# Kernel optimization log

Measured on AMD Instinct MI355X. Metric: run time of the kernel, lower is better.

The kernel has to match this reference:

```python
import jax, jax.numpy as jnp
import numpy as np

VOCAB = 50257
EMBED = 256
NFREQ = 64
NRULES = 100
B, S = 4, 1024


def setup_inputs() -> dict:
    key = jax.random.key(0)
    ks = jax.random.split(key, 7)
    return {
        "token_ids": jax.random.randint(ks[0], (B, S), 0, VOCAB),
        "a_n": jax.random.normal(ks[1], (VOCAB, NFREQ), dtype=jnp.float32),
        "b_n": jax.random.normal(ks[2], (VOCAB, NFREQ), dtype=jnp.float32),
        "rule_transform": jax.random.normal(ks[3], (NRULES, EMBED, EMBED), dtype=jnp.float32),
        "token_rules": jax.random.randint(ks[4], (VOCAB,), 0, NRULES),
        "proj_w": jax.random.normal(ks[5], (EMBED, NFREQ), dtype=jnp.float32) * (1.0 / np.sqrt(NFREQ)),
        "proj_b": jax.random.normal(ks[6], (EMBED,), dtype=jnp.float32) * 0.01,
    }


def reference(token_ids, a_n, b_n, rule_transform, token_rules, proj_w, proj_b):
    vocab_size, nfreq = a_n.shape
    # fourier_freqs = linspace(1, F, F) -> [1..F]
    freqs = jnp.arange(1, nfreq + 1, dtype=jnp.float32)  # [F]
    x = token_ids.astype(jnp.float32)[..., None] / vocab_size  # [B,S,1]
    ang = (2.0 * jnp.pi) * freqs * x  # [B,S,F]
    # gather per-token fourier coefficients, fuse cos/sin combine
    fourier = a_n[token_ids] * jnp.cos(ang) + b_n[token_ids] * jnp.sin(ang)  # [B,S,F]
    base = jnp.einsum('bsf,df->bsd', fourier, proj_w) + proj_b  # [B,S,D]
    rule_idx = token_rules[token_ids]  # [B,S]
    rules = rule_transform[rule_idx]  # [B,S,D,D] gathered per token
    return jnp.einsum('bsd,bsde->bse', base, rules)  # [B,S,D]
```

## Files before the change

### kernel.cpp

```cpp
#include <hip/hip_runtime.h>
#include <math.h>

#define VOCAB   50257
#define EMBED   256
#define NFREQ   64
#define NRULES  100
#define NTOK    4096
#define CAP     256
#define CHUNK   16
#define NCHUNK  (CAP / CHUNK)

#define BASE_BYTES ((size_t)NTOK * EMBED * 4)
#define LIST_BYTES ((size_t)NRULES * CAP * 4)

__global__ __launch_bounds__(256) void prep_kernel(
    const float* __restrict__ proj_w,
    float*       __restrict__ wT,
    int*         __restrict__ counts)
{
    __shared__ float s_t[64 * 65];
    const int tid = threadIdx.x;
    const int b   = blockIdx.x;

    if (b == 0 && tid < NRULES) counts[tid] = 0;

    const float4* __restrict__ W4 =
        (const float4*)(proj_w + (size_t)b * 64 * NFREQ);
    #pragma unroll
    for (int i = 0; i < 4; ++i) {
        const int v = i * 256 + tid;
        const float4 w = W4[v];
        const int dl = v >> 4, f0 = (v & 15) * 4;
        s_t[dl * 65 + f0 + 0] = w.x;
        s_t[dl * 65 + f0 + 1] = w.y;
        s_t[dl * 65 + f0 + 2] = w.z;
        s_t[dl * 65 + f0 + 3] = w.w;
    }
    __syncthreads();
    #pragma unroll
    for (int j = 0; j < 16; ++j) {
        const int o = j * 256 + tid;
        const int f = o >> 6, c = o & 63;
        wT[f * EMBED + b * 64 + c] = s_t[c * 65 + f];
    }
}

__global__ __launch_bounds__(256) void fused_base_kernel(
    const int*   __restrict__ token_ids,
    const float* __restrict__ a_n,
    const float* __restrict__ b_n,
    const int*   __restrict__ token_rules,
    const float* __restrict__ wT,
    const float* __restrict__ proj_b,
    float*       __restrict__ base,
    int*         __restrict__ counts,
    int*         __restrict__ list)
{
    __shared__ float s_four[4][NFREQ];

    const int tid = threadIdx.x;
    const int tl  = tid >> 6;
    const int f   = tid & 63;
    const int tok_idx = blockIdx.x * 4 + tl;
    const int tok     = token_ids[tok_idx];

    const float x   = (float)tok * (1.0f / (float)VOCAB);
    const float rev = (float)(f + 1) * x;
    const float rf  = rev - floorf(rev);
    const float sv  = __builtin_amdgcn_sinf(rf);
    const float cv  = __builtin_amdgcn_cosf(rf);
    s_four[tl][f] = a_n[(size_t)tok * NFREQ + f] * cv
                  + b_n[(size_t)tok * NFREQ + f] * sv;

    if (f == 0) {
        const int rule = token_rules[tok];
        const int pos  = atomicAdd(&counts[rule], 1);
        if (pos < CAP) list[rule * CAP + pos] = tok_idx;
    }
    __syncthreads();

    const int   d    = tid;
    const float bias = proj_b[d];
    float a0 = bias, a1 = bias, a2 = bias, a3 = bias;

    #pragma unroll 4
    for (int q = 0; q < 16; ++q) {
        const float w0 = wT[(4 * q + 0) * EMBED + d];
        const float w1 = wT[(4 * q + 1) * EMBED + d];
        const float w2 = wT[(4 * q + 2) * EMBED + d];
        const float w3 = wT[(4 * q + 3) * EMBED + d];
        const float4 f0 = ((const float4*)s_four[0])[q];
        const float4 f1 = ((const float4*)s_four[1])[q];
        const float4 f2 = ((const float4*)s_four[2])[q];
        const float4 f3 = ((const float4*)s_four[3])[q];
        a0 += w0 * f0.x + w1 * f0.y + w2 * f0.z + w3 * f0.w;
        a1 += w0 * f1.x + w1 * f1.y + w2 * f1.z + w3 * f1.w;
        a2 += w0 * f2.x + w1 * f2.y + w2 * f2.z + w3 * f2.w;
        a3 += w0 * f3.x + w1 * f3.y + w2 * f3.z + w3 * f3.w;
    }
    base[(size_t)(blockIdx.x * 4 + 0) * EMBED + d] = a0;
    base[(size_t)(blockIdx.x * 4 + 1) * EMBED + d] = a1;
    base[(size_t)(blockIdx.x * 4 + 2) * EMBED + d] = a2;
    base[(size_t)(blockIdx.x * 4 + 3) * EMBED + d] = a3;
}

__global__ __launch_bounds__(512) void apply_kernel(
    const float* __restrict__ base,
    const float* __restrict__ rule_transform,
    const int*   __restrict__ counts,
    const int*   __restrict__ list,
    float*       __restrict__ out)
{
    __shared__ float s_stage[8 * CHUNK * 64];
    __shared__ float s_part[6 * CHUNK * 128];

    const int rule = blockIdx.x;
    int cnt = counts[rule];
    if (cnt > CAP) cnt = CAP;
    const int t0 = blockIdx.y * CHUNK;
    if (t0 >= cnt) return;

    const int tid  = threadIdx.x;
    const int w8   = tid >> 6;
    const int ds   = w8 >> 1;
    const int eh   = w8 & 1;
    const int lane = tid & 63;
    const int d0   = ds * 64;

    const int* __restrict__ lst = list + rule * CAP;

    int idx[CHUNK];
    #pragma unroll
    for (int t = 0; t < CHUNK; ++t) {
        int tt = t0 + t;
        if (tt > cnt - 1) tt = cnt - 1;
        idx[t] = __builtin_amdgcn_readfirstlane(lst[tt]);
    }

    float* my_stage = s_stage + w8 * (CHUNK * 64);
    #pragma unroll
    for (int t = 0; t < CHUNK; ++t)
        my_stage[t * 64 + lane] = base[(size_t)idx[t] * EMBED + d0 + lane];

    const float2* __restrict__ T2 =
        (const float2*)(rule_transform + (size_t)rule * EMBED * EMBED);
    const int ec = eh * 64 + lane;

    float2 acc[CHUNK];
    #pragma unroll
    for (int t = 0; t < CHUNK; ++t) { acc[t].x = 0.f; acc[t].y = 0.f; }

    float2 tv0[4], tv1[4], tv2[4], tvn[4];
    #pragma unroll
    for (int i = 0; i < 4; ++i) tv0[i] = T2[(size_t)(d0 + i) * 128 + ec];
    #pragma unroll
    for (int i = 0; i < 4; ++i) tv1[i] = T2[(size_t)(d0 + 4 + i) * 128 + ec];
    #pragma unroll
    for (int i = 0; i < 4; ++i) tv2[i] = T2[(size_t)(d0 + 8 + i) * 128 + ec];

    for (int dq = 0; dq < 16; ++dq) {
        if (dq < 13) {
            #pragma unroll
            for (int i = 0; i < 4; ++i)
                tvn[i] = T2[(size_t)(d0 + (dq + 3) * 4 + i) * 128 + ec];
        }
        #pragma unroll
        for (int t = 0; t < CHUNK; ++t) {
            const float4 b4 = *(const float4*)&my_stage[t * 64 + dq * 4];
            acc[t].x += b4.x * tv0[0].x + b4.y * tv0[1].x
                      + b4.z * tv0[2].x + b4.w * tv0[3].x;
            acc[t].y += b4.x * tv0[0].y + b4.y * tv0[1].y
                      + b4.z * tv0[2].y + b4.w * tv0[3].y;
        }
        #pragma unroll
        for (int i = 0; i < 4; ++i) {
            tv0[i] = tv1[i]; tv1[i] = tv2[i]; tv2[i] = tvn[i];
        }
    }

    if (ds > 0) {
        float2* dst = (float2*)(s_part + ((ds - 1) * 2 + eh) * (CHUNK * 128));
        #pragma unroll
        for (int t = 0; t < CHUNK; ++t) dst[t * 64 + lane] = acc[t];
    }
    __syncthreads();
    if (ds == 0) {
        #pragma unroll
        for (int t = 0; t < CHUNK; ++t) {
            #pragma unroll
            for (int r = 0; r < 3; ++r) {
                const float2 p = ((const float2*)
                    (s_part + (r * 2 + eh) * (CHUNK * 128)))[t * 64 + lane];
                acc[t].x += p.x; acc[t].y += p.y;
            }
            if (t0 + t < cnt)
                *(float2*)&out[(size_t)idx[t] * EMBED + eh * 128 + lane * 2]
                    = acc[t];
        }
    }
}

extern "C" void kernel_launch(void* const* d_in, const int* in_sizes, int n_in,
                              void* d_out, int out_size, void* d_ws, size_t ws_size,
                              hipStream_t stream) {
    const int*   token_ids      = (const int*)  d_in[0];
    const float* a_n            = (const float*)d_in[1];
    const float* b_n            = (const float*)d_in[2];
    const float* rule_transform = (const float*)d_in[3];
    const int*   token_rules    = (const int*)  d_in[4];
    const float* proj_w         = (const float*)d_in[5];
    const float* proj_b         = (const float*)d_in[6];
    float*       out            = (float*)d_out;

    float* base   = (float*)d_ws;
    int*   counts = (int*)((char*)d_ws + BASE_BYTES);
    int*   list   = (int*)((char*)d_ws + BASE_BYTES + 512);
    float* wT     = (float*)((char*)d_ws + BASE_BYTES + 512 + LIST_BYTES);

    prep_kernel<<<4, 256, 0, stream>>>(proj_w, wT, counts);
    fused_base_kernel<<<NTOK / 4, 256, 0, stream>>>(
        token_ids, a_n, b_n, token_rules, wT, proj_b, base, counts, list);
    apply_kernel<<<dim3(NRULES, NCHUNK), 512, 0, stream>>>(
        base, rule_transform, counts, list, out);
}
```

Measured before the change: 130.6 us.

## Use bf16 MFMA for per-rule transform with pre-swizzled bf16 rule matrices

Result: faster. 124.8 us (-4.5%).

```diff
diff --git a/kernel.cpp b/kernel.cpp
--- a/kernel.cpp
+++ b/kernel.cpp
@@ -8,15 +8,27 @@
 #define NTOK    4096
 #define CAP     256
 #define CHUNK   16
-#define NCHUNK  (CAP / CHUNK)
-
-#define BASE_BYTES ((size_t)NTOK * EMBED * 4)
-#define LIST_BYTES ((size_t)NRULES * CAP * 4)
+#define NCHUNK  8
+
+typedef __attribute__((ext_vector_type(8))) short short8;
+typedef __attribute__((ext_vector_type(4))) float floatx4;
+
+#define BASEBF_BYTES ((size_t)NTOK * EMBED * 2)
+#define LIST_BYTES   ((size_t)NRULES * CAP * 4)
+#define CNT_OFF      (BASEBF_BYTES)
+#define LIST_OFF     (CNT_OFF + 512)
+#define WT_OFF       (LIST_OFF + LIST_BYTES)
+#define TFRAG_OFF    (WT_OFF + (size_t)NFREQ * EMBED * 4)
+
+__device__ __forceinline__ ushort f2bf(float f) {
+    unsigned u = __float_as_uint(f);
+    unsigned r = (u + 0x7FFFu + ((u >> 16) & 1u)) >> 16;
+    return (ushort)r;
+}
 
 __global__ __launch_bounds__(256) void prep_kernel(
-    const float* __restrict__ proj_w,
-    float*       __restrict__ wT,
-    int*         __restrict__ counts)
+    const float* __restrict__ proj_w, float* __restrict__ wT,
+    int* __restrict__ counts)
 {
     __shared__ float s_t[64 * 65];
     const int tid = threadIdx.x;
@@ -45,6 +57,44 @@
     }
 }
 
+__global__ __launch_bounds__(256) void convert_kernel(
+    const float* __restrict__ T,
+    ushort*      __restrict__ Tfrag)
+{
+    __shared__ float s[32 * 260];
+    const int tid = threadIdx.x;
+    const int r   = blockIdx.x;
+    const int kb  = blockIdx.y;
+
+    const float4* __restrict__ src =
+        (const float4*)(T + (size_t)r * 65536 + (size_t)kb * 32 * 256);
+    #pragma unroll
+    for (int i = 0; i < 8; ++i) {
+        const int v   = i * 256 + tid;
+        const int row = v >> 6, c4 = v & 63;
+        ((float4*)s)[row * 65 + c4] = src[v];
+    }
+    __syncthreads();
+
+    const int et  = tid >> 4;
+    const int l16 = tid & 15;
+    uint4* __restrict__ dst = (uint4*)Tfrag + (size_t)r * 16384;
+
+    #pragma unroll
+    for (int lg = 0; lg < 4; ++lg) {
+        ushort h[8];
+        #pragma unroll
+        for (int j = 0; j < 8; ++j)
+            h[j] = f2bf(s[(lg * 8 + j) * 260 + et * 16 + l16]);
+        uint4 o;
+        o.x = (unsigned)h[0] | ((unsigned)h[1] << 16);
+        o.y = (unsigned)h[2] | ((unsigned)h[3] << 16);
+        o.z = (unsigned)h[4] | ((unsigned)h[5] << 16);
+        o.w = (unsigned)h[6] | ((unsigned)h[7] << 16);
+        dst[(et * 8 + kb) * 64 + lg * 16 + l16] = o;
+    }
+}
+
 __global__ __launch_bounds__(256) void fused_base_kernel(
     const int*   __restrict__ token_ids,
     const float* __restrict__ a_n,
@@ -52,7 +102,7 @@
     const int*   __restrict__ token_rules,
     const float* __restrict__ wT,
     const float* __restrict__ proj_b,
-    float*       __restrict__ base,
+    ushort*      __restrict__ base_bf,
     int*         __restrict__ counts,
     int*         __restrict__ list)
 {
@@ -98,21 +148,20 @@
         a2 += w0 * f2.x + w1 * f2.y + w2 * f2.z + w3 * f2.w;
         a3 += w0 * f3.x + w1 * f3.y + w2 * f3.z + w3 * f3.w;
     }
-    base[(size_t)(blockIdx.x * 4 + 0) * EMBED + d] = a0;
-    base[(size_t)(blockIdx.x * 4 + 1) * EMBED + d] = a1;
-    base[(size_t)(blockIdx.x * 4 + 2) * EMBED + d] = a2;
-    base[(size_t)(blockIdx.x * 4 + 3) * EMBED + d] = a3;
-}
-
-__global__ __launch_bounds__(512) void apply_kernel(
-    const float* __restrict__ base,
-    const float* __restrict__ rule_transform,
-    const int*   __restrict__ counts,
-    const int*   __restrict__ list,
-    float*       __restrict__ out)
-{
-    __shared__ float s_stage[8 * CHUNK * 64];
-    __shared__ float s_part[6 * CHUNK * 128];
+    base_bf[(size_t)(blockIdx.x * 4 + 0) * EMBED + d] = f2bf(a0);
+    base_bf[(size_t)(blockIdx.x * 4 + 1) * EMBED + d] = f2bf(a1);
+    base_bf[(size_t)(blockIdx.x * 4 + 2) * EMBED + d] = f2bf(a2);
+    base_bf[(size_t)(blockIdx.x * 4 + 3) * EMBED + d] = f2bf(a3);
+}
+
+__global__ __launch_bounds__(256) void apply_kernel(
+    const ushort* __restrict__ base_bf,
+    const ushort* __restrict__ Tfrag,
+    const int*    __restrict__ counts,
+    const int*    __restrict__ list,
+    float*        __restrict__ out)
+{
+    __shared__ __align__(16) ushort s_a[16 * 264];
 
     const int rule = blockIdx.x;
     int cnt = counts[rule];
@@ -121,14 +170,10 @@
     if (t0 >= cnt) return;
 
     const int tid  = threadIdx.x;
-    const int w8   = tid >> 6;
-    const int ds   = w8 >> 1;
-    const int eh   = w8 & 1;
+    const int w    = tid >> 6;
     const int lane = tid & 63;
-    const int d0   = ds * 64;
 
     const int* __restrict__ lst = list + rule * CAP;
-
     int idx[CHUNK];
     #pragma unroll
     for (int t = 0; t < CHUNK; ++t) {
@@ -137,65 +182,54 @@
         idx[t] = __builtin_amdgcn_readfirstlane(lst[tt]);
     }
 
-    float* my_stage = s_stage + w8 * (CHUNK * 64);
-    #pragma unroll
-    for (int t = 0; t < CHUNK; ++t)
-        my_stage[t * 64 + lane] = base[(size_t)idx[t] * EMBED + d0 + lane];
-
-    const float2* __restrict__ T2 =
-        (const float2*)(rule_transform + (size_t)rule * EMBED * EMBED);
-    const int ec = eh * 64 + lane;
-
-    float2 acc[CHUNK];
-    #pragma unroll
-    for (int t = 0; t < CHUNK; ++t) { acc[t].x = 0.f; acc[t].y = 0.f; }
-
-    float2 tv0[4], tv1[4], tv2[4], tvn[4];
-    #pragma unroll
-    for (int i = 0; i < 4; ++i) tv0[i] = T2[(size_t)(d0 + i) * 128 + ec];
-    #pragma unroll
-    for (int i = 0; i < 4; ++i) tv1[i] = T2[(size_t)(d0 + 4 + i) * 128 + ec];
-    #pragma unroll
-    for (int i = 0; i < 4; ++i) tv2[i] = T2[(size_t)(d0 + 8 + i) * 128 + ec];
-
-    for (int dq = 0; dq < 16; ++dq) {
-        if (dq < 13) {
+    #pragma unroll
+    for (int i = 0; i < 2; ++i) {
+        const int v = i * 256 + tid;
+        const int t = v >> 5, c = v & 31;
+        ((uint4*)s_a)[t * 33 + c * 2 / 2] =
+            ((const uint4*)(base_bf + (size_t)idx[t] * EMBED))[c];
+    }
+    __syncthreads();
+
+    const short8* __restrict__ Bf =
+        (const short8*)Tfrag + (size_t)rule * 16384;
+
+    floatx4 acc[4];
+    #pragma unroll
+    for (int q = 0; q < 4; ++q) acc[q] = (floatx4){0.f, 0.f, 0.f, 0.f};
+
+    const int arow = (lane & 15) * 33 + (lane >> 4);
+
+    short8 bcur[4], bnxt[4];
+    #pragma unroll
+    for (int q = 0; q < 4; ++q)
+        bcur[q] = Bf[((w * 4 + q) * 8 + 0) * 64 + lane];
+
+    for (int kb = 0; kb < 8; ++kb) {
+        if (kb < 7) {
             #pragma unroll
-            for (int i = 0; i < 4; ++i)
-                tvn[i] = T2[(size_t)(d0 + (dq + 3) * 4 + i) * 128 + ec];
+            for (int q = 0; q < 4; ++q)
+                bnxt[q] = Bf[((w * 4 + q) * 8 + kb + 1) * 64 + lane];
         }
-        #pragma unroll
-        for (int t = 0; t < CHUNK; ++t) {
-            const float4 b4 = *(const float4*)&my_stage[t * 64 + dq * 4];
-            acc[t].x += b4.x * tv0[0].x + b4.y * tv0[1].x
-                      + b4.z * tv0[2].x + b4.w * tv0[3].x;
-            acc[t].y += b4.x * tv0[0].y + b4.y * tv0[1].y
-                      + b4.z * tv0[2].y + b4.w * tv0[3].y;
-        }
-        #pragma unroll
-        for (int i = 0; i < 4; ++i) {
-            tv0[i] = tv1[i]; tv1[i] = tv2[i]; tv2[i] = tvn[i];
-        }
-    }
-
-    if (ds > 0) {
-        float2* dst = (float2*)(s_part + ((ds - 1) * 2 + eh) * (CHUNK * 128));
-        #pragma unroll
-        for (int t = 0; t < CHUNK; ++t) dst[t * 64 + lane] = acc[t];
-    }
-    __syncthreads();
-    if (ds == 0) {
-        #pragma unroll
-        for (int t = 0; t < CHUNK; ++t) {
-            #pragma unroll
-            for (int r = 0; r < 3; ++r) {
-                const float2 p = ((const float2*)
-                    (s_part + (r * 2 + eh) * (CHUNK * 128)))[t * 64 + lane];
-                acc[t].x += p.x; acc[t].y += p.y;
-            }
-            if (t0 + t < cnt)
-                *(float2*)&out[(size_t)idx[t] * EMBED + eh * 128 + lane * 2]
-                    = acc[t];
+        const short8 av = ((const short8*)s_a)[arow + kb * 4];
+        #pragma unroll
+        for (int q = 0; q < 4; ++q)
+            acc[q] = __builtin_amdgcn_mfma_f32_16x16x32_bf16(
+                av, bcur[q], acc[q], 0, 0, 0);
+        #pragma unroll
+        for (int q = 0; q < 4; ++q) bcur[q] = bnxt[q];
+    }
+
+    const int m4 = (lane >> 4) * 4;
+    const int n  = lane & 15;
+    #pragma unroll
+    for (int q = 0; q < 4; ++q) {
+        const int e = (w * 4 + q) * 16 + n;
+        #pragma unroll
+        for (int r = 0; r < 4; ++r) {
+            const int m = m4 + r;
+            if (t0 + m < cnt)
+                out[(size_t)idx[m] * EMBED + e] = acc[q][r];
         }
     }
 }
@@ -212,14 +246,16 @@
     const float* proj_b         = (const float*)d_in[6];
     float*       out            = (float*)d_out;
 
-    float* base   = (float*)d_ws;
-    int*   counts = (int*)((char*)d_ws + BASE_BYTES);
-    int*   list   = (int*)((char*)d_ws + BASE_BYTES + 512);
-    float* wT     = (float*)((char*)d_ws + BASE_BYTES + 512 + LIST_BYTES);
+    ushort* base_bf = (ushort*)d_ws;
+    int*    counts  = (int*)   ((char*)d_ws + CNT_OFF);
+    int*    list    = (int*)   ((char*)d_ws + LIST_OFF);
+    float*  wT      = (float*) ((char*)d_ws + WT_OFF);
+    ushort* Tfrag   = (ushort*)((char*)d_ws + TFRAG_OFF);
 
     prep_kernel<<<4, 256, 0, stream>>>(proj_w, wT, counts);
+    convert_kernel<<<dim3(NRULES, 8), 256, 0, stream>>>(rule_transform, Tfrag);
     fused_base_kernel<<<NTOK / 4, 256, 0, stream>>>(
-        token_ids, a_n, b_n, token_rules, wT, proj_b, base, counts, list);
-    apply_kernel<<<dim3(NRULES, NCHUNK), 512, 0, stream>>>(
-        base, rule_transform, counts, list, out);
-}
+        token_ids, a_n, b_n, token_rules, wT, proj_b, base_bf, counts, list);
+    apply_kernel<<<dim3(NRULES, NCHUNK), 256, 0, stream>>>(
+        base_bf, Tfrag, counts, list, out);
+}
```
